# Kernel optimization log

Measured on AMD Instinct MI355X. Metric: run time of the kernel, lower is better.

The kernel has to match this reference:

```python
import jax, jax.numpy as jnp
import numpy as np

DIM = 1024
N_HEADS = 16
N_KV = 4
HEAD_DIM = 64
FFN = 4096
EPS = 1e-6
B, S = 2, 2048
ROPE_BASE = 10000.0


def rmsnorm(x, w, eps=EPS):
    ms = jnp.mean(jnp.square(x), axis=-1, keepdims=True)
    return x * jax.lax.rsqrt(ms + eps) * w


def apply_rotary(x, cos, sin):
    # x: [B,H,S,hd]; cos/sin: [S, hd//2] -> broadcast over B,H
    half = x.shape[-1] // 2
    x1, x2 = x[..., :half], x[..., half:]
    c = cos[None, None, :, :]
    s = sin[None, None, :, :]
    return jnp.concatenate((x1 * c + x2 * s, x2 * c - x1 * s), axis=-1)


def setup_inputs() -> dict:
    key = jax.random.key(0)
    ks = jax.random.split(key, 10)
    w = lambda k, shp: jax.random.normal(k, shp, dtype=jnp.float32) * 0.02
    pos = jnp.arange(S, dtype=jnp.float32)
    inv_freq = 1.0 / (ROPE_BASE ** (jnp.arange(0, HEAD_DIM // 2, dtype=jnp.float32) / (HEAD_DIM // 2)))
    ang = pos[:, None] * inv_freq[None, :]
    return {
        "x": jax.random.normal(ks[0], (B, S, DIM), dtype=jnp.float32),
        "w_norm1": jnp.ones((DIM,), jnp.float32),
        "wq": w(ks[1], (DIM, N_HEADS * HEAD_DIM)),
        "wk": w(ks[2], (DIM, N_KV * HEAD_DIM)),
        "wv": w(ks[3], (DIM, N_KV * HEAD_DIM)),
        "wo": w(ks[4], (N_HEADS * HEAD_DIM, DIM)),
        "attn_scale": jnp.ones((DIM,), jnp.float32),
        "w_norm2": jnp.ones((DIM,), jnp.float32),
        "wg": w(ks[5], (DIM, FFN)),
        "wu": w(ks[6], (DIM, FFN)),
        "wd": w(ks[7], (FFN, DIM)),
        "mlp_scale": jnp.ones((DIM,), jnp.float32),
        "cos": jnp.cos(ang),
        "sin": jnp.sin(ang),
    }


def block_forward(x, w_norm1, wq, wk, wv, wo, attn_scale, w_norm2, wg, wu, wd, mlp_scale, cos, sin):
    b, s, d = x.shape
    # ---- attention sub-block (pre-norm, RoPE, causal GQA SDPA, scaled residual) ----
    xn = rmsnorm(x, w_norm1)
    q = (xn @ wq).reshape(b, s, N_HEADS, HEAD_DIM).transpose(0, 2, 1, 3)  # [B,H,S,hd]
    k = (xn @ wk).reshape(b, s, N_KV, HEAD_DIM).transpose(0, 2, 1, 3)    # [B,KV,S,hd]
    v = (xn @ wv).reshape(b, s, N_KV, HEAD_DIM).transpose(0, 2, 1, 3)
    q = apply_rotary(q, cos, sin)
    k = apply_rotary(k, cos, sin)
    rep = N_HEADS // N_KV
    k = jnp.repeat(k, rep, axis=1)  # GQA expand -> [B,H,S,hd]
    v = jnp.repeat(v, rep, axis=1)
    scale = 1.0 / np.sqrt(HEAD_DIM)
    scores = jnp.einsum("bhqd,bhkd->bhqk", q, k) * scale
    causal = jnp.tril(jnp.ones((s, s), dtype=bool))
    scores = jnp.where(causal[None, None], scores, jnp.finfo(scores.dtype).min)
    probs = jax.nn.softmax(scores, axis=-1)
    attn = jnp.einsum("bhqk,bhkd->bhqd", probs, v)
    attn = attn.transpose(0, 2, 1, 3).reshape(b, s, N_HEADS * HEAD_DIM)
    x = x + (attn @ wo) * attn_scale[None, None, :]
    # ---- MLP sub-block (pre-norm, fused gate/up SwiGLU, down proj, scaled residual) ----
    xn2 = rmsnorm(x, w_norm2)
    hidden = jax.nn.silu(xn2 @ wg) * (xn2 @ wu)  # SwiGLU
    x = x + (hidden @ wd) * mlp_scale[None, None, :]
    return x


def reference(x, w_norm1, wq, wk, wv, wo, attn_scale, w_norm2, wg, wu, wd, mlp_scale, cos, sin):
    return block_forward(x, w_norm1, wq, wk, wv, wo, attn_scale, w_norm2, wg, wu, wd, mlp_scale, cos, sin)
```

## Files before the change

kernel.cpp:

```cpp
#include <hip/hip_runtime.h>
#include <hip/hip_bf16.h>
#include <cstdint>

typedef unsigned short u16;
typedef __attribute__((ext_vector_type(4))) float f32x4;
typedef __attribute__((ext_vector_type(8))) __bf16 bf16x8;

#define NH 16
#define NKV 4
#define SEQ 2048
#define NTOK 4096

__device__ inline u16 f2bf(float f) {
  return __builtin_bit_cast(u16, __float2bfloat16(f));
}
__device__ inline float bf2f(u16 u) {
  return __bfloat162float(__builtin_bit_cast(__hip_bfloat16, u));
}

#define GLDS(gp, lp) __builtin_amdgcn_global_load_lds( \
    (__attribute__((address_space(1))) void*)(gp), \
    (__attribute__((address_space(3))) void*)(lp), 16, 0, 0)

#define VMCNT0 asm volatile("s_waitcnt vmcnt(0)" ::: "memory")

__global__ __launch_bounds__(256) void rmsnorm_kernel(
    const float* __restrict__ x, const float* __restrict__ w,
    u16* __restrict__ out) {
  int row = blockIdx.x;
  int tid = threadIdx.x;
  const float4 v = reinterpret_cast<const float4*>(x + (size_t)row * 1024)[tid];
  float ss = v.x * v.x + v.y * v.y + v.z * v.z + v.w * v.w;
#pragma unroll
  for (int off = 32; off; off >>= 1) ss += __shfl_xor(ss, off);
  __shared__ float red[4];
  int lane = tid & 63, wid = tid >> 6;
  if (lane == 0) red[wid] = ss;
  __syncthreads();
  float tot = red[0] + red[1] + red[2] + red[3];
  float r = rsqrtf(tot * (1.0f / 1024.0f) + 1e-6f);
  const float4 wv = reinterpret_cast<const float4*>(w)[tid];
  ushort4 o;
  o.x = f2bf(v.x * r * wv.x);
  o.y = f2bf(v.y * r * wv.y);
  o.z = f2bf(v.z * r * wv.z);
  o.w = f2bf(v.w * r * wv.w);
  reinterpret_cast<ushort4*>(out + (size_t)row * 1024)[tid] = o;
}

__global__ __launch_bounds__(256) void transpose_cast_kernel(
    const float* __restrict__ src, u16* __restrict__ dst, int K, int N) {
  __shared__ float tile[32][33];
  int n0 = blockIdx.x * 32, k0 = blockIdx.y * 32;
  int tx = threadIdx.x & 31, ty = threadIdx.x >> 5;
#pragma unroll
  for (int i = 0; i < 4; i++)
    tile[ty + i * 8][tx] = src[(size_t)(k0 + ty + i * 8) * N + n0 + tx];
  __syncthreads();
#pragma unroll
  for (int i = 0; i < 4; i++)
    dst[(size_t)(n0 + ty + i * 8) * K + k0 + tx] = f2bf(tile[tx][ty + i * 8]);
}

template <int EP>
__device__ inline void epi_store(float v, size_t idx, int col,
                                 float* __restrict__ outf,
                                 const float* __restrict__ res,
                                 const float* __restrict__ scale,
                                 u16* __restrict__ outb) {
  if (EP == 0) {
    outf[idx] = v;
  } else if (EP == 1) {
    outf[idx] = res[idx] + v * scale[col];
  } else if (EP == 2) {
    outb[idx] = f2bf(v / (1.0f + __expf(-v)));
  } else {
    outb[idx] = f2bf(bf2f(outb[idx]) * v);
  }
}

template <int EP>
__global__ __launch_bounds__(512, 1) void gemmA(
    const u16* __restrict__ A, const u16* __restrict__ Bt,
    int M, int N, int K,
    float* __restrict__ outf, const float* __restrict__ res,
    const float* __restrict__ scale, u16* __restrict__ outb) {
  __shared__ u16 SA[2][256 * 64];
  __shared__ u16 SB[2][256 * 64];
  const int tid = threadIdx.x, lane = tid & 63, w = tid >> 6;
  const int wr = w >> 2, wc = w & 3;
  const int lg = lane >> 4, lc = lane & 15, cx = lc & 7;

  const int nbn = N >> 8;
  const int r8 = blockIdx.x & 7, j = blockIdx.x >> 3;
  const int bm = (((r8 >> 1) << 2) + (j & 3)) << 8;
  const int bn = ((r8 & 1) * (nbn >> 1) + (j >> 2)) << 8;

  const int swrow = lane >> 3;
  const int swcol = (lane & 7) ^ swrow;
  const u16* gA = A + (size_t)(bm + w * 16 + swrow) * K + swcol * 8;
  const u16* gB = Bt + (size_t)(bn + w * 16 + swrow) * K + swcol * 8;

  const int NT = K >> 6;
  f32x4 acc[8][4] = {};

#define SGA(T_) do { int sl_ = (T_) & 1; size_t ko_ = (size_t)(T_) * 64; \
    GLDS(gA + ko_,                    &SA[sl_][(w * 16) * 64]); \
    GLDS(gA + ko_ + (size_t)8 * K,    &SA[sl_][(w * 16 + 8) * 64]); \
    GLDS(gA + ko_ + (size_t)128 * K,  &SA[sl_][(128 + w * 16) * 64]); \
    GLDS(gA + ko_ + (size_t)136 * K,  &SA[sl_][(136 + w * 16) * 64]); } while (0)
#define SGB(T_) do { int sl_ = (T_) & 1; size_t ko_ = (size_t)(T_) * 64; \
    GLDS(gB + ko_,                    &SB[sl_][(w * 16) * 64]); \
    GLDS(gB + ko_ + (size_t)8 * K,    &SB[sl_][(w * 16 + 8) * 64]); \
    GLDS(gB + ko_ + (size_t)128 * K,  &SB[sl_][(128 + w * 16) * 64]); \
    GLDS(gB + ko_ + (size_t)136 * K,  &SB[sl_][(136 + w * 16) * 64]); } while (0)

  SGA(0);
  SGB(0);
  VMCNT0;
  __builtin_amdgcn_s_barrier();

  for (int t = 0; t < NT; ++t) {
    const u16* sa = &SA[t & 1][0];
    const u16* sb = &SB[t & 1][0];
    const bool more = (t + 1 < NT);

    bf16x8 bfr[4][2];
#pragma unroll
    for (int n = 0; n < 4; n++) {
      const int row = wc * 64 + n * 16 + lc;
#pragma unroll
      for (int ks = 0; ks < 2; ks++)
        bfr[n][ks] = *reinterpret_cast<const bf16x8*>(
            &sb[row * 64 + ((((ks << 2) | lg) ^ cx) << 3)]);
    }
    bf16x8 afr[4][2];
#pragma unroll
    for (int i = 0; i < 4; i++) {
      const int row = wr * 128 + i * 16 + lc;
#pragma unroll
      for (int ks = 0; ks < 2; ks++)
        afr[i][ks] = *reinterpret_cast<const bf16x8*>(
            &sa[row * 64 + ((((ks << 2) | lg) ^ cx) << 3)]);
    }
    if (more) SGA(t + 1);
    __builtin_amdgcn_s_setprio(1);
#pragma unroll
    for (int i = 0; i < 4; i++)
#pragma unroll
      for (int n = 0; n < 4; n++) {
        acc[i][n] = __builtin_amdgcn_mfma_f32_16x16x32_bf16(afr[i][0], bfr[n][0], acc[i][n], 0, 0, 0);
        acc[i][n] = __builtin_amdgcn_mfma_f32_16x16x32_bf16(afr[i][1], bfr[n][1], acc[i][n], 0, 0, 0);
      }
    __builtin_amdgcn_s_setprio(0);
#pragma unroll
    for (int i = 0; i < 4; i++) {
      const int row = wr * 128 + 64 + i * 16 + lc;
#pragma unroll
      for (int ks = 0; ks < 2; ks++)
        afr[i][ks] = *reinterpret_cast<const bf16x8*>(
            &sa[row * 64 + ((((ks << 2) | lg) ^ cx) << 3)]);
    }
    if (more) SGB(t + 1);
    __builtin_amdgcn_s_setprio(1);
#pragma unroll
    for (int i = 0; i < 4; i++)
#pragma unroll
      for (int n = 0; n < 4; n++) {
        acc[4 + i][n] = __builtin_amdgcn_mfma_f32_16x16x32_bf16(afr[i][0], bfr[n][0], acc[4 + i][n], 0, 0, 0);
        acc[4 + i][n] = __builtin_amdgcn_mfma_f32_16x16x32_bf16(afr[i][1], bfr[n][1], acc[4 + i][n], 0, 0, 0);
      }
    __builtin_amdgcn_s_setprio(0);
    VMCNT0;
    __builtin_amdgcn_s_barrier();
  }
#undef SGA
#undef SGB

#pragma unroll
  for (int mi = 0; mi < 8; mi++)
#pragma unroll
    for (int ni = 0; ni < 4; ni++)
#pragma unroll
      for (int rg = 0; rg < 4; rg++) {
        const int row = bm + wr * 128 + mi * 16 + lg * 4 + rg;
        const int col = bn + wc * 64 + ni * 16 + lc;
        epi_store<EP>(acc[mi][ni][rg], (size_t)row * N + col, col, outf, res, scale, outb);
      }
}

template <int EP>
__global__ __launch_bounds__(256, 1) void gemmB(
    const u16* __restrict__ A, const u16* __restrict__ Bt,
    int M, int N, int K,
    float* __restrict__ outf, const float* __restrict__ res,
    const float* __restrict__ scale, u16* __restrict__ outb) {
  __shared__ u16 SA[2][128 * 64];
  __shared__ u16 SB[2][128 * 64];
  const int tid = threadIdx.x, lane = tid & 63, w = tid >> 6;
  const int wr = w >> 1, wc = w & 1;
  const int lg = lane >> 4, lc = lane & 15, cx = lc & 7;

  const int r8 = blockIdx.x & 7, j = blockIdx.x >> 3;
  const int bm = ((r8 << 2) + (j & 3)) << 7;
  const int bn = (j >> 2) << 7;

  const int swrow = lane >> 3;
  const int swcol = (lane & 7) ^ swrow;
  const u16* gA = A + (size_t)(bm + w * 32 + swrow) * K + swcol * 8;
  const u16* gB = Bt + (size_t)(bn + w * 32 + swrow) * K + swcol * 8;

  const int NT = K >> 6;
  f32x4 acc[4][4] = {};

#define SG2(T_) do { int sl_ = (T_) & 1; size_t ko_ = (size_t)(T_) * 64; \
    GLDS(gA + ko_,                   &SA[sl_][(w * 32) * 64]); \
    GLDS(gA + ko_ + (size_t)8 * K,   &SA[sl_][(w * 32 + 8) * 64]); \
    GLDS(gA + ko_ + (size_t)16 * K,  &SA[sl_][(w * 32 + 16) * 64]); \
    GLDS(gA + ko_ + (size_t)24 * K,  &SA[sl_][(w * 32 + 24) * 64]); \
    GLDS(gB + ko_,                   &SB[sl_][(w * 32) * 64]); \
    GLDS(gB + ko_ + (size_t)8 * K,   &SB[sl_][(w * 32 + 8) * 64]); \
    GLDS(gB + ko_ + (size_t)16 * K,  &SB[sl_][(w * 32 + 16) * 64]); \
    GLDS(gB + ko_ + (size_t)24 * K,  &SB[sl_][(w * 32 + 24) * 64]); } while (0)

  SG2(0);
  VMCNT0;
  __builtin_amdgcn_s_barrier();

  for (int t = 0; t < NT; ++t) {
    const u16* sa = &SA[t & 1][0];
    const u16* sb = &SB[t & 1][0];
    const bool more = (t + 1 < NT);

    bf16x8 bfr[4][2], afr[4][2];
#pragma unroll
    for (int n = 0; n < 4; n++) {
      const int row = wc * 64 + n * 16 + lc;
#pragma unroll
      for (int ks = 0; ks < 2; ks++)
        bfr[n][ks] = *reinterpret_cast<const bf16x8*>(
            &sb[row * 64 + ((((ks << 2) | lg) ^ cx) << 3)]);
    }
#pragma unroll
    for (int i = 0; i < 4; i++) {
      const int row = wr * 64 + i * 16 + lc;
#pragma unroll
      for (int ks = 0; ks < 2; ks++)
        afr[i][ks] = *reinterpret_cast<const bf16x8*>(
            &sa[row * 64 + ((((ks << 2) | lg) ^ cx) << 3)]);
    }
    if (more) SG2(t + 1);
    __builtin_amdgcn_s_setprio(1);
#pragma unroll
    for (int i = 0; i < 4; i++)
#pragma unroll
      for (int n = 0; n < 4; n++) {
        acc[i][n] = __builtin_amdgcn_mfma_f32_16x16x32_bf16(afr[i][0], bfr[n][0], acc[i][n], 0, 0, 0);
        acc[i][n] = __builtin_amdgcn_mfma_f32_16x16x32_bf16(afr[i][1], bfr[n][1], acc[i][n], 0, 0, 0);
      }
    __builtin_amdgcn_s_setprio(0);
    VMCNT0;
    __builtin_amdgcn_s_barrier();
  }
#undef SG2

#pragma unroll
  for (int mi = 0; mi < 4; mi++)
#pragma unroll
    for (int ni = 0; ni < 4; ni++)
#pragma unroll
      for (int rg = 0; rg < 4; rg++) {
        const int row = bm + wr * 64 + mi * 16 + lg * 4 + rg;
        const int col = bn + wc * 64 + ni * 16 + lc;
        epi_store<EP>(acc[mi][ni][rg], (size_t)row * N + col, col, outf, res, scale, outb);
      }
}

__global__ __launch_bounds__(256) void rope_kernel(
    const float* __restrict__ qkv, const float* __restrict__ cosb,
    const float* __restrict__ sinb, u16* __restrict__ qr, u16* __restrict__ kr) {
  int idx = blockIdx.x * 256 + threadIdx.x;
  int d = idx & 31;
  int t = idx >> 5;
  int head = t % 20;
  int bs = t / 20;
  int s = bs & (SEQ - 1);
  int b = bs >> 11;
  const float* row = qkv + (size_t)bs * 1536;
  float c = cosb[s * 32 + d], sn = sinb[s * 32 + d];
  const float QSC = 0.18033688011112042f;
  float x1, x2;
  if (head < 16) {
    x1 = row[head * 64 + d];
    x2 = row[head * 64 + d + 32];
    size_t o = ((size_t)(b * NH + head) * SEQ + s) * 64 + d;
    qr[o] = f2bf((x1 * c + x2 * sn) * QSC);
    qr[o + 32] = f2bf((x2 * c - x1 * sn) * QSC);
  } else {
    int kh = head - 16;
    x1 = row[1024 + kh * 64 + d];
    x2 = row[1024 + kh * 64 + d + 32];
    size_t o = ((size_t)(b * NKV + kh) * SEQ + s) * 64 + d;
    kr[o] = f2bf(x1 * c + x2 * sn);
    kr[o + 32] = f2bf(x2 * c - x1 * sn);
  }
}

__global__ __launch_bounds__(256) void vtrans_kernel(
    const float* __restrict__ qkv, u16* __restrict__ vt) {
  int blk = blockIdx.x;
  int st = blk & 31; blk >>= 5;
  int kvh = blk & 3; blk >>= 2;
  int b = blk;
  __shared__ u16 tile[64][65];
  int tx = threadIdx.x & 63;
  int ty = threadIdx.x >> 6;
  int s0 = st * 64;
#pragma unroll
  for (int i = 0; i < 16; i++) {
    int sl = i * 4 + ty;
    tile[sl][tx] = f2bf(qkv[(size_t)(b * SEQ + s0 + sl) * 1536 + 1280 + kvh * 64 + tx]);
  }
  __syncthreads();
  size_t vbase = (size_t)(b * NKV + kvh) * 64 * SEQ;
#pragma unroll
  for (int i = 0; i < 16; i++) {
    int dd = i * 4 + ty;
    vt[vbase + (size_t)dd * SEQ + s0 + tx] = tile[tx][dd];
  }
}

__global__ __launch_bounds__(512, 1) void attn_kernel(
    const u16* __restrict__ qr, const u16* __restrict__ kr,
    const u16* __restrict__ vt, u16* __restrict__ out) {
  __shared__ u16 Ks[2][64 * 64];
  __shared__ u16 Vs[2][64 * 64];
  __shared__ u16 Ps[8][32 * 64];

  const int n = blockIdx.x;
  const int g = n & 7;
  const int b = g >> 2, kvh = g & 3;
  const int h = kvh * 4 + ((n >> 3) & 3);
  const int j = n >> 5;

  const int tid = threadIdx.x;
  const int lane = tid & 63, w = tid >> 6;
  const int lg = lane >> 4, lc = lane & 15;
  const int lc7 = lc & 7;

  const int isH = (w ^ (w >> 2)) & 1;
  const int strip = isH ? (15 - j) : j;
  const int q0w = strip * 128 + (w >> 1) * 32;
  const int nt = 2 * (15 - j) + 2;

  bf16x8 qf[2][2];
  {
    const u16* qp = qr + ((size_t)(b * NH + h) * SEQ + q0w + lc) * 64 + lg * 8;
#pragma unroll
    for (int qt = 0; qt < 2; qt++) {
      qf[qt][0] = *reinterpret_cast<const bf16x8*>(qp + qt * 16 * 64);
      qf[qt][1] = *reinterpret_cast<const bf16x8*>(qp + qt * 16 * 64 + 32);
    }
  }
  VMCNT0;

  const int srow = lane >> 3;
  const int scw = ((lane & 7) ^ srow) << 3;
  const u16* ksrc = kr + (size_t)(b * NKV + kvh) * SEQ * 64 + (size_t)(w * 8 + srow) * 64 + scw;
  const u16* vsrc = vt + ((size_t)(b * NKV + kvh) * 64 + w * 8 + srow) * SEQ + scw;
  u16* Pw = &Ps[w][0];

#define STAGEA(bufi, t) do { \
    GLDS(ksrc + (size_t)(t) * 64 * 64, &Ks[bufi][(w * 8) * 64]); \
    GLDS(vsrc + (size_t)(t) * 64,      &Vs[bufi][(w * 8) * 64]); \
  } while (0)

  STAGEA(0, 0);

  float mm[2] = {-1e30f, -1e30f}, ll[2] = {0.0f, 0.0f};
  f32x4 oacc[2][4] = {};

  int buf = 0;
  for (int t = 0; t < nt; ++t) {
    if (t + 1 < nt) {
      STAGEA(buf ^ 1, t + 1);
      asm volatile("s_waitcnt vmcnt(2)" ::: "memory");
    } else {
      VMCNT0;
    }
    __builtin_amdgcn_s_barrier();
    __builtin_amdgcn_sched_barrier(0);

    const int c0 = t * 64;
    if (c0 <= q0w + 31) {
      bf16x8 kf[4][2];
#pragma unroll
      for (int ni = 0; ni < 4; ni++) {
        const int row = ni * 16 + lc;
#pragma unroll
        for (int hf = 0; hf < 2; hf++)
          kf[ni][hf] = *reinterpret_cast<const bf16x8*>(
              &Ks[buf][row * 64 + ((((hf * 64 + lg * 16)) ^ (lc7 << 4)) >> 1)]);
      }
      f32x4 sc[4][2] = {};
      __builtin_amdgcn_s_setprio(1);
#pragma unroll
      for (int ni = 0; ni < 4; ni++)
#pragma unroll
        for (int qt = 0; qt < 2; qt++) {
          sc[ni][qt] = __builtin_amdgcn_mfma_f32_16x16x32_bf16(kf[ni][0], qf[qt][0], sc[ni][qt], 0, 0, 0);
          sc[ni][qt] = __builtin_amdgcn_mfma_f32_16x16x32_bf16(kf[ni][1], qf[qt][1], sc[ni][qt], 0, 0, 0);
        }
      __builtin_amdgcn_s_setprio(0);
      bf16x8 vf[4][2];
#pragma unroll
      for (int dt = 0; dt < 4; dt++) {
        const int row = dt * 16 + lc;
#pragma unroll
        for (int ks = 0; ks < 2; ks++)
          vf[dt][ks] = *reinterpret_cast<const bf16x8*>(
              &Vs[buf][row * 64 + (((ks * 64 + lg * 16) ^ (lc7 << 4)) >> 1)]);
      }
      if (c0 + 63 > q0w) {
#pragma unroll
        for (int qt = 0; qt < 2; qt++) {
          const int q = q0w + qt * 16 + lc;
#pragma unroll
          for (int ni = 0; ni < 4; ni++)
#pragma unroll
            for (int rg = 0; rg < 4; rg++)
              if (c0 + ni * 16 + lg * 4 + rg > q) sc[ni][qt][rg] = -1e30f;
        }
      }
      float mx[2];
#pragma unroll
      for (int qt = 0; qt < 2; qt++) {
        float v = -1e30f;
#pragma unroll
        for (int ni = 0; ni < 4; ni++)
#pragma unroll
          for (int rg = 0; rg < 4; rg++) v = fmaxf(v, sc[ni][qt][rg]);
        v = fmaxf(v, __shfl_xor(v, 16));
        v = fmaxf(v, __shfl_xor(v, 32));
        mx[qt] = v;
      }
      if (!__all(mx[0] - mm[0] <= 11.5f && mx[1] - mm[1] <= 11.5f)) {
        float al[2];
#pragma unroll
        for (int qt = 0; qt < 2; qt++) {
          float mn = fmaxf(mm[qt], mx[qt]);
          al[qt] = exp2f(mm[qt] - mn);
          mm[qt] = mn;
          ll[qt] *= al[qt];
        }
#pragma unroll
        for (int qt = 0; qt < 2; qt++)
#pragma unroll
          for (int rg = 0; rg < 4; rg++) {
            float a = __shfl(al[qt], lg * 4 + rg);
#pragma unroll
            for (int dt = 0; dt < 4; dt++) oacc[qt][dt][rg] *= a;
          }
      }
#pragma unroll
      for (int qt = 0; qt < 2; qt++) {
        float rs = 0.0f;
#pragma unroll
        for (int ni = 0; ni < 4; ni++)
#pragma unroll
          for (int rg = 0; rg < 4; rg++) {
            float p = exp2f(sc[ni][qt][rg] - mm[qt]);
            sc[ni][qt][rg] = p;
            rs += p;
          }
        rs += __shfl_xor(rs, 16);
        rs += __shfl_xor(rs, 32);
        ll[qt] += rs;
      }
#pragma unroll
      for (int qt = 0; qt < 2; qt++)
#pragma unroll
        for (int ni = 0; ni < 4; ni++) {
          ushort4 pk;
          pk.x = f2bf(sc[ni][qt][0]);
          pk.y = f2bf(sc[ni][qt][1]);
          pk.z = f2bf(sc[ni][qt][2]);
          pk.w = f2bf(sc[ni][qt][3]);
          *reinterpret_cast<ushort4*>(
              &Pw[(qt * 16 + lc) * 64 + (((ni * 32 + lg * 8) ^ (lc7 << 4)) >> 1)]) = pk;
        }
      __builtin_amdgcn_s_setprio(1);
#pragma unroll
      for (int qt = 0; qt < 2; qt++)
#pragma unroll
        for (int ks = 0; ks < 2; ks++) {
          bf16x8 pa = *reinterpret_cast<const bf16x8*>(
              &Pw[(qt * 16 + lc) * 64 + (((ks * 64 + lg * 16) ^ (lc7 << 4)) >> 1)]);
#pragma unroll
          for (int dt = 0; dt < 4; dt++)
            oacc[qt][dt] = __builtin_amdgcn_mfma_f32_16x16x32_bf16(pa, vf[dt][ks], oacc[qt][dt], 0, 0, 0);
        }
      __builtin_amdgcn_s_setprio(0);
    }
    asm volatile("s_waitcnt lgkmcnt(0)" ::: "memory");
    __builtin_amdgcn_s_barrier();
    __builtin_amdgcn_sched_barrier(0);
    buf ^= 1;
  }
#undef STAGEA

#pragma unroll
  for (int qt = 0; qt < 2; qt++) {
    const float li = 1.0f / ll[qt];
#pragma unroll
    for (int rg = 0; rg < 4; rg++) {
      float liq = __shfl(li, lg * 4 + rg);
      int q = q0w + qt * 16 + lg * 4 + rg;
      u16* orow = out + (size_t)(b * SEQ + q) * 1024 + h * 64 + lc;
#pragma unroll
      for (int dt = 0; dt < 4; dt++)
        orow[dt * 16] = f2bf(oacc[qt][dt][rg] * liq);
    }
  }
}

extern "C" void kernel_launch(void* const* d_in, const int* in_sizes, int n_in,
                              void* d_out, int out_size, void* d_ws, size_t ws_size,
                              hipStream_t stream) {
  const float* x = (const float*)d_in[0];
  const float* w_norm1 = (const float*)d_in[1];
  const float* wq = (const float*)d_in[2];
  const float* wk = (const float*)d_in[3];
  const float* wv = (const float*)d_in[4];
  const float* wo = (const float*)d_in[5];
  const float* attn_scale = (const float*)d_in[6];
  const float* w_norm2 = (const float*)d_in[7];
  const float* wg = (const float*)d_in[8];
  const float* wu = (const float*)d_in[9];
  const float* wd = (const float*)d_in[10];
  const float* mlp_scale = (const float*)d_in[11];
  const float* cosb = (const float*)d_in[12];
  const float* sinb = (const float*)d_in[13];
  float* out = (float*)d_out;

  char* ws = (char*)d_ws;
  u16* wqkv_t = (u16*)(ws + 0);
  u16* wo_t = (u16*)(ws + 3145728);
  u16* wg_t = (u16*)(ws + 5242880);
  u16* wu_t = (u16*)(ws + 13631488);
  u16* wd_t = (u16*)(ws + 22020096);
  u16* xn = (u16*)(ws + 30408704);
  float* qkv = (float*)(ws + 38797312);
  u16* attn_o = (u16*)(ws + 38797312);
  float* x1 = (float*)(ws + 47185920);
  u16* q_rope = (u16*)(ws + 63963136);
  u16* k_rope = (u16*)(ws + 72351744);
  u16* vt = (u16*)(ws + 74448896);
  u16* hbuf = (u16*)(ws + 63963136);

  dim3 tb(256);
  transpose_cast_kernel<<<dim3(32, 32), tb, 0, stream>>>(wq, wqkv_t, 1024, 1024);
  transpose_cast_kernel<<<dim3(8, 32), tb, 0, stream>>>(wk, wqkv_t + (size_t)1024 * 1024, 1024, 256);
  transpose_cast_kernel<<<dim3(8, 32), tb, 0, stream>>>(wv, wqkv_t + (size_t)1280 * 1024, 1024, 256);
  transpose_cast_kernel<<<dim3(32, 32), tb, 0, stream>>>(wo, wo_t, 1024, 1024);
  transpose_cast_kernel<<<dim3(128, 32), tb, 0, stream>>>(wg, wg_t, 1024, 4096);
  transpose_cast_kernel<<<dim3(128, 32), tb, 0, stream>>>(wu, wu_t, 1024, 4096);
  transpose_cast_kernel<<<dim3(32, 128), tb, 0, stream>>>(wd, wd_t, 4096, 1024);

  rmsnorm_kernel<<<4096, tb, 0, stream>>>(x, w_norm1, xn);
  gemmB<0><<<dim3(384), dim3(256), 0, stream>>>(xn, wqkv_t, 4096, 1536, 1024, qkv, nullptr, nullptr, nullptr);
  rope_kernel<<<10240, tb, 0, stream>>>(qkv, cosb, sinb, q_rope, k_rope);
  vtrans_kernel<<<2 * 4 * 32, tb, 0, stream>>>(qkv, vt);
  attn_kernel<<<256, dim3(512), 0, stream>>>(q_rope, k_rope, vt, attn_o);
  gemmB<1><<<dim3(256), dim3(256), 0, stream>>>(attn_o, wo_t, 4096, 1024, 1024, x1, x, attn_scale, nullptr);
  rmsnorm_kernel<<<4096, tb, 0, stream>>>(x1, w_norm2, xn);
  gemmA<2><<<dim3(256), dim3(512), 0, stream>>>(xn, wg_t, 4096, 4096, 1024, nullptr, nullptr, nullptr, hbuf);
  gemmA<3><<<dim3(256), dim3(512), 0, stream>>>(xn, wu_t, 4096, 4096, 1024, nullptr, nullptr, nullptr, hbuf);
  gemmB<1><<<dim3(256), dim3(256), 0, stream>>>(hbuf, wd_t, 4096, 1024, 4096, out, x1, mlp_scale, nullptr);
}
```

Baseline: 284.0 us.

## Switch attention to 32x32x16 MFMA and keep P in registers

Rewrites the attention inner loop to use 32x32x16 bf16 MFMA tiles instead of 16x16x32. With that tiling each lane owns a single query row, so the softmax state collapses to one max and one sum per lane. The probability matrix is repacked into the A-operand layout with cross-half lane shuffles, which removes the per-wave LDS scratch buffer and its write/read round trip. This trades LDS traffic and bank pressure for extra shuffles, more accumulator registers and a reworked mask and output index mapping that must match the MFMA layout exactly.

```diff
diff --git a/kernel.cpp b/kernel.cpp
--- a/kernel.cpp
+++ b/kernel.cpp
@@ -3,7 +3,9 @@
 #include <cstdint>
 
 typedef unsigned short u16;
+typedef unsigned int u32;
 typedef __attribute__((ext_vector_type(4))) float f32x4;
+typedef __attribute__((ext_vector_type(16))) float f32x16;
 typedef __attribute__((ext_vector_type(8))) __bf16 bf16x8;
 
 #define NH 16
@@ -16,6 +18,9 @@
 }
 __device__ inline float bf2f(u16 u) {
   return __bfloat162float(__builtin_bit_cast(__hip_bfloat16, u));
+}
+__device__ inline u32 pk2(float a, float b) {
+  return (u32)f2bf(a) | ((u32)f2bf(b) << 16);
 }
 
 #define GLDS(gp, lp) __builtin_amdgcn_global_load_lds( \
@@ -335,7 +340,6 @@
     const u16* __restrict__ vt, u16* __restrict__ out) {
   __shared__ u16 Ks[2][64 * 64];
   __shared__ u16 Vs[2][64 * 64];
-  __shared__ u16 Ps[8][32 * 64];
 
   const int n = blockIdx.x;
   const int g = n & 7;
@@ -345,22 +349,20 @@
 
   const int tid = threadIdx.x;
   const int lane = tid & 63, w = tid >> 6;
-  const int lg = lane >> 4, lc = lane & 15;
-  const int lc7 = lc & 7;
+  const int l31 = lane & 31, hi = lane >> 5;
 
   const int isH = (w ^ (w >> 2)) & 1;
   const int strip = isH ? (15 - j) : j;
   const int q0w = strip * 128 + (w >> 1) * 32;
+  const int qg = q0w + l31;
   const int nt = 2 * (15 - j) + 2;
 
-  bf16x8 qf[2][2];
+  bf16x8 qf[4];
   {
-    const u16* qp = qr + ((size_t)(b * NH + h) * SEQ + q0w + lc) * 64 + lg * 8;
-#pragma unroll
-    for (int qt = 0; qt < 2; qt++) {
-      qf[qt][0] = *reinterpret_cast<const bf16x8*>(qp + qt * 16 * 64);
-      qf[qt][1] = *reinterpret_cast<const bf16x8*>(qp + qt * 16 * 64 + 32);
-    }
+    const u16* qp = qr + ((size_t)(b * NH + h) * SEQ + qg) * 64 + 8 * hi;
+#pragma unroll
+    for (int c = 0; c < 4; c++)
+      qf[c] = *reinterpret_cast<const bf16x8*>(qp + 16 * c);
   }
   VMCNT0;
 
@@ -368,7 +370,6 @@
   const int scw = ((lane & 7) ^ srow) << 3;
   const u16* ksrc = kr + (size_t)(b * NKV + kvh) * SEQ * 64 + (size_t)(w * 8 + srow) * 64 + scw;
   const u16* vsrc = vt + ((size_t)(b * NKV + kvh) * 64 + w * 8 + srow) * SEQ + scw;
-  u16* Pw = &Ps[w][0];
 
 #define STAGEA(bufi, t) do { \
     GLDS(ksrc + (size_t)(t) * 64 * 64, &Ks[bufi][(w * 8) * 64]); \
@@ -377,8 +378,8 @@
 
   STAGEA(0, 0);
 
-  float mm[2] = {-1e30f, -1e30f}, ll[2] = {0.0f, 0.0f};
-  f32x4 oacc[2][4] = {};
+  float mm = -1e30f, ll = 0.0f;
+  f32x16 oacc[2] = {};
 
   int buf = 0;
   for (int t = 0; t < nt; ++t) {
@@ -393,113 +394,100 @@
 
     const int c0 = t * 64;
     if (c0 <= q0w + 31) {
-      bf16x8 kf[4][2];
-#pragma unroll
-      for (int ni = 0; ni < 4; ni++) {
-        const int row = ni * 16 + lc;
-#pragma unroll
-        for (int hf = 0; hf < 2; hf++)
-          kf[ni][hf] = *reinterpret_cast<const bf16x8*>(
-              &Ks[buf][row * 64 + ((((hf * 64 + lg * 16)) ^ (lc7 << 4)) >> 1)]);
-      }
-      f32x4 sc[4][2] = {};
+      f32x16 sc[2] = {};
       __builtin_amdgcn_s_setprio(1);
 #pragma unroll
-      for (int ni = 0; ni < 4; ni++)
-#pragma unroll
-        for (int qt = 0; qt < 2; qt++) {
-          sc[ni][qt] = __builtin_amdgcn_mfma_f32_16x16x32_bf16(kf[ni][0], qf[qt][0], sc[ni][qt], 0, 0, 0);
-          sc[ni][qt] = __builtin_amdgcn_mfma_f32_16x16x32_bf16(kf[ni][1], qf[qt][1], sc[ni][qt], 0, 0, 0);
+      for (int a = 0; a < 2; a++) {
+        const int row = a * 32 + l31;
+#pragma unroll
+        for (int c = 0; c < 4; c++) {
+          bf16x8 kf = *reinterpret_cast<const bf16x8*>(
+              &Ks[buf][row * 64 + (((2 * c + hi) ^ (row & 7)) << 3)]);
+          sc[a] = __builtin_amdgcn_mfma_f32_32x32x16_bf16(kf, qf[c], sc[a], 0, 0, 0);
         }
+      }
       __builtin_amdgcn_s_setprio(0);
-      bf16x8 vf[4][2];
-#pragma unroll
-      for (int dt = 0; dt < 4; dt++) {
-        const int row = dt * 16 + lc;
-#pragma unroll
-        for (int ks = 0; ks < 2; ks++)
-          vf[dt][ks] = *reinterpret_cast<const bf16x8*>(
-              &Vs[buf][row * 64 + (((ks * 64 + lg * 16) ^ (lc7 << 4)) >> 1)]);
-      }
+
+      bf16x8 vf[2][4];
+#pragma unroll
+      for (int dch = 0; dch < 2; dch++) {
+        const int row = dch * 32 + l31;
+#pragma unroll
+        for (int c = 0; c < 4; c++)
+          vf[dch][c] = *reinterpret_cast<const bf16x8*>(
+              &Vs[buf][row * 64 + (((2 * c + hi) ^ (row & 7)) << 3)]);
+      }
+
       if (c0 + 63 > q0w) {
 #pragma unroll
-        for (int qt = 0; qt < 2; qt++) {
-          const int q = q0w + qt * 16 + lc;
-#pragma unroll
-          for (int ni = 0; ni < 4; ni++)
-#pragma unroll
-            for (int rg = 0; rg < 4; rg++)
-              if (c0 + ni * 16 + lg * 4 + rg > q) sc[ni][qt][rg] = -1e30f;
+        for (int a = 0; a < 2; a++)
+#pragma unroll
+          for (int r = 0; r < 16; r++) {
+            const int key = c0 + 32 * a + (r & 3) + 8 * (r >> 2) + 4 * hi;
+            if (key > qg) sc[a][r] = -1e30f;
+          }
+      }
+
+      float mx = -1e30f;
+#pragma unroll
+      for (int a = 0; a < 2; a++)
+#pragma unroll
+        for (int r = 0; r < 16; r++) mx = fmaxf(mx, sc[a][r]);
+      mx = fmaxf(mx, __shfl_xor(mx, 32));
+
+      if (!__all(mx - mm <= 11.5f)) {
+        float mn = fmaxf(mm, mx);
+        float al = exp2f(mm - mn);
+        mm = mn;
+        ll *= al;
+#pragma unroll
+        for (int r = 0; r < 16; r++) {
+          float arr = __shfl(al, (r & 3) + 8 * (r >> 2) + 4 * hi);
+          oacc[0][r] *= arr;
+          oacc[1][r] *= arr;
         }
       }
-      float mx[2];
-#pragma unroll
-      for (int qt = 0; qt < 2; qt++) {
-        float v = -1e30f;
-#pragma unroll
-        for (int ni = 0; ni < 4; ni++)
-#pragma unroll
-          for (int rg = 0; rg < 4; rg++) v = fmaxf(v, sc[ni][qt][rg]);
-        v = fmaxf(v, __shfl_xor(v, 16));
-        v = fmaxf(v, __shfl_xor(v, 32));
-        mx[qt] = v;
-      }
-      if (!__all(mx[0] - mm[0] <= 11.5f && mx[1] - mm[1] <= 11.5f)) {
-        float al[2];
-#pragma unroll
-        for (int qt = 0; qt < 2; qt++) {
-          float mn = fmaxf(mm[qt], mx[qt]);
-          al[qt] = exp2f(mm[qt] - mn);
-          mm[qt] = mn;
-          ll[qt] *= al[qt];
+
+      float rs = 0.0f;
+#pragma unroll
+      for (int a = 0; a < 2; a++)
+#pragma unroll
+        for (int r = 0; r < 16; r++) {
+          float p = exp2f(sc[a][r] - mm);
+          sc[a][r] = p;
+          rs += p;
         }
-#pragma unroll
-        for (int qt = 0; qt < 2; qt++)
-#pragma unroll
-          for (int rg = 0; rg < 4; rg++) {
-            float a = __shfl(al[qt], lg * 4 + rg);
-#pragma unroll
-            for (int dt = 0; dt < 4; dt++) oacc[qt][dt][rg] *= a;
-          }
-      }
-#pragma unroll
-      for (int qt = 0; qt < 2; qt++) {
-        float rs = 0.0f;
-#pragma unroll
-        for (int ni = 0; ni < 4; ni++)
-#pragma unroll
-          for (int rg = 0; rg < 4; rg++) {
-            float p = exp2f(sc[ni][qt][rg] - mm[qt]);
-            sc[ni][qt][rg] = p;
-            rs += p;
-          }
-        rs += __shfl_xor(rs, 16);
-        rs += __shfl_xor(rs, 32);
-        ll[qt] += rs;
-      }
-#pragma unroll
-      for (int qt = 0; qt < 2; qt++)
-#pragma unroll
-        for (int ni = 0; ni < 4; ni++) {
-          ushort4 pk;
-          pk.x = f2bf(sc[ni][qt][0]);
-          pk.y = f2bf(sc[ni][qt][1]);
-          pk.z = f2bf(sc[ni][qt][2]);
-          pk.w = f2bf(sc[ni][qt][3]);
-          *reinterpret_cast<ushort4*>(
-              &Pw[(qt * 16 + lc) * 64 + (((ni * 32 + lg * 8) ^ (lc7 << 4)) >> 1)]) = pk;
-        }
+      rs += __shfl_xor(rs, 32);
+      ll += rs;
+
+      bf16x8 pa[4];
+#pragma unroll
+      for (int c = 0; c < 4; c++) {
+        const int a = c >> 1;
+        const int bb = 8 * (c & 1);
+        u32 A0 = pk2(sc[a][bb + 0], sc[a][bb + 1]);
+        u32 A1 = pk2(sc[a][bb + 2], sc[a][bb + 3]);
+        u32 B0 = pk2(sc[a][bb + 4], sc[a][bb + 5]);
+        u32 B1 = pk2(sc[a][bb + 6], sc[a][bb + 7]);
+        u32 s0 = hi ? A0 : B0;
+        u32 s1 = hi ? A1 : B1;
+        u32 r0 = (u32)__shfl_xor((int)s0, 32);
+        u32 r1 = (u32)__shfl_xor((int)s1, 32);
+        u32 w0 = hi ? r0 : A0;
+        u32 w1 = hi ? r1 : A1;
+        u32 w2 = hi ? B0 : r0;
+        u32 w3 = hi ? B1 : r1;
+        uint4 pw;
+        pw.x = w0; pw.y = w1; pw.z = w2; pw.w = w3;
+        pa[c] = __builtin_bit_cast(bf16x8, pw);
+      }
+
       __builtin_amdgcn_s_setprio(1);
 #pragma unroll
-      for (int qt = 0; qt < 2; qt++)
-#pragma unroll
-        for (int ks = 0; ks < 2; ks++) {
-          bf16x8 pa = *reinterpret_cast<const bf16x8*>(
-              &Pw[(qt * 16 + lc) * 64 + (((ks * 64 + lg * 16) ^ (lc7 << 4)) >> 1)]);
-#pragma unroll
-          for (int dt = 0; dt < 4; dt++)
-            oacc[qt][dt] = __builtin_amdgcn_mfma_f32_16x16x32_bf16(pa, vf[dt][ks], oacc[qt][dt], 0, 0, 0);
-        }
+      for (int c = 0; c < 4; c++) {
+        oacc[0] = __builtin_amdgcn_mfma_f32_32x32x16_bf16(pa[c], vf[0][c], oacc[0], 0, 0, 0);
+        oacc[1] = __builtin_amdgcn_mfma_f32_32x32x16_bf16(pa[c], vf[1][c], oacc[1], 0, 0, 0);
+      }
       __builtin_amdgcn_s_setprio(0);
     }
     asm volatile("s_waitcnt lgkmcnt(0)" ::: "memory");
@@ -509,18 +497,15 @@
   }
 #undef STAGEA
 
-#pragma unroll
-  for (int qt = 0; qt < 2; qt++) {
-    const float li = 1.0f / ll[qt];
-#pragma unroll
-    for (int rg = 0; rg < 4; rg++) {
-      float liq = __shfl(li, lg * 4 + rg);
-      int q = q0w + qt * 16 + lg * 4 + rg;
-      u16* orow = out + (size_t)(b * SEQ + q) * 1024 + h * 64 + lc;
-#pragma unroll
-      for (int dt = 0; dt < 4; dt++)
-        orow[dt * 16] = f2bf(oacc[qt][dt][rg] * liq);
-    }
+  const float li = 1.0f / ll;
+#pragma unroll
+  for (int r = 0; r < 16; r++) {
+    const int qloc = (r & 3) + 8 * (r >> 2) + 4 * hi;
+    float liq = __shfl(li, qloc);
+    const int q = q0w + qloc;
+    u16* orow = out + (size_t)(b * SEQ + q) * 1024 + h * 64 + l31;
+    orow[0] = f2bf(oacc[0][r] * liq);
+    orow[32] = f2bf(oacc[1][r] * liq);
   }
 }
 
```

After: 284.9 us. About the same (+0.3%).

## Fuse gate and up projections into one SwiGLU GEMM kernel

Applied to the files above, without the earlier changes.

Replaces the two separate gate and up GEMM launches, the second of which re-read and rewrote the bf16 hidden buffer, with one kernel that computes both accumulators from a shared A tile and applies SiLU(g)*u in the epilogue. This removes one full read of the activation matrix, the intermediate bf16 round-trip of the gate output, and one launch. Tiles change to 256x128 with K-step 32 and 2 blocks per CU, and each wave now holds two accumulator sets. The smaller K step doubles the barrier count per K, and register pressure may limit occupancy.

```diff
diff --git a/kernel.cpp b/kernel.cpp
--- a/kernel.cpp
+++ b/kernel.cpp
@@ -3,6 +3,7 @@
 #include <cstdint>
 
 typedef unsigned short u16;
+typedef unsigned int u32;
 typedef __attribute__((ext_vector_type(4))) float f32x4;
 typedef __attribute__((ext_vector_type(8))) __bf16 bf16x8;
 
@@ -80,116 +81,6 @@
 }
 
 template <int EP>
-__global__ __launch_bounds__(512, 1) void gemmA(
-    const u16* __restrict__ A, const u16* __restrict__ Bt,
-    int M, int N, int K,
-    float* __restrict__ outf, const float* __restrict__ res,
-    const float* __restrict__ scale, u16* __restrict__ outb) {
-  __shared__ u16 SA[2][256 * 64];
-  __shared__ u16 SB[2][256 * 64];
-  const int tid = threadIdx.x, lane = tid & 63, w = tid >> 6;
-  const int wr = w >> 2, wc = w & 3;
-  const int lg = lane >> 4, lc = lane & 15, cx = lc & 7;
-
-  const int nbn = N >> 8;
-  const int r8 = blockIdx.x & 7, j = blockIdx.x >> 3;
-  const int bm = (((r8 >> 1) << 2) + (j & 3)) << 8;
-  const int bn = ((r8 & 1) * (nbn >> 1) + (j >> 2)) << 8;
-
-  const int swrow = lane >> 3;
-  const int swcol = (lane & 7) ^ swrow;
-  const u16* gA = A + (size_t)(bm + w * 16 + swrow) * K + swcol * 8;
-  const u16* gB = Bt + (size_t)(bn + w * 16 + swrow) * K + swcol * 8;
-
-  const int NT = K >> 6;
-  f32x4 acc[8][4] = {};
-
-#define SGA(T_) do { int sl_ = (T_) & 1; size_t ko_ = (size_t)(T_) * 64; \
-    GLDS(gA + ko_,                    &SA[sl_][(w * 16) * 64]); \
-    GLDS(gA + ko_ + (size_t)8 * K,    &SA[sl_][(w * 16 + 8) * 64]); \
-    GLDS(gA + ko_ + (size_t)128 * K,  &SA[sl_][(128 + w * 16) * 64]); \
-    GLDS(gA + ko_ + (size_t)136 * K,  &SA[sl_][(136 + w * 16) * 64]); } while (0)
-#define SGB(T_) do { int sl_ = (T_) & 1; size_t ko_ = (size_t)(T_) * 64; \
-    GLDS(gB + ko_,                    &SB[sl_][(w * 16) * 64]); \
-    GLDS(gB + ko_ + (size_t)8 * K,    &SB[sl_][(w * 16 + 8) * 64]); \
-    GLDS(gB + ko_ + (size_t)128 * K,  &SB[sl_][(128 + w * 16) * 64]); \
-    GLDS(gB + ko_ + (size_t)136 * K,  &SB[sl_][(136 + w * 16) * 64]); } while (0)
-
-  SGA(0);
-  SGB(0);
-  VMCNT0;
-  __builtin_amdgcn_s_barrier();
-
-  for (int t = 0; t < NT; ++t) {
-    const u16* sa = &SA[t & 1][0];
-    const u16* sb = &SB[t & 1][0];
-    const bool more = (t + 1 < NT);
-
-    bf16x8 bfr[4][2];
-#pragma unroll
-    for (int n = 0; n < 4; n++) {
-      const int row = wc * 64 + n * 16 + lc;
-#pragma unroll
-      for (int ks = 0; ks < 2; ks++)
-        bfr[n][ks] = *reinterpret_cast<const bf16x8*>(
-            &sb[row * 64 + ((((ks << 2) | lg) ^ cx) << 3)]);
-    }
-    bf16x8 afr[4][2];
-#pragma unroll
-    for (int i = 0; i < 4; i++) {
-      const int row = wr * 128 + i * 16 + lc;
-#pragma unroll
-      for (int ks = 0; ks < 2; ks++)
-        afr[i][ks] = *reinterpret_cast<const bf16x8*>(
-            &sa[row * 64 + ((((ks << 2) | lg) ^ cx) << 3)]);
-    }
-    if (more) SGA(t + 1);
-    __builtin_amdgcn_s_setprio(1);
-#pragma unroll
-    for (int i = 0; i < 4; i++)
-#pragma unroll
-      for (int n = 0; n < 4; n++) {
-        acc[i][n] = __builtin_amdgcn_mfma_f32_16x16x32_bf16(afr[i][0], bfr[n][0], acc[i][n], 0, 0, 0);
-        acc[i][n] = __builtin_amdgcn_mfma_f32_16x16x32_bf16(afr[i][1], bfr[n][1], acc[i][n], 0, 0, 0);
-      }
-    __builtin_amdgcn_s_setprio(0);
-#pragma unroll
-    for (int i = 0; i < 4; i++) {
-      const int row = wr * 128 + 64 + i * 16 + lc;
-#pragma unroll
-      for (int ks = 0; ks < 2; ks++)
-        afr[i][ks] = *reinterpret_cast<const bf16x8*>(
-            &sa[row * 64 + ((((ks << 2) | lg) ^ cx) << 3)]);
-    }
-    if (more) SGB(t + 1);
-    __builtin_amdgcn_s_setprio(1);
-#pragma unroll
-    for (int i = 0; i < 4; i++)
-#pragma unroll
-      for (int n = 0; n < 4; n++) {
-        acc[4 + i][n] = __builtin_amdgcn_mfma_f32_16x16x32_bf16(afr[i][0], bfr[n][0], acc[4 + i][n], 0, 0, 0);
-        acc[4 + i][n] = __builtin_amdgcn_mfma_f32_16x16x32_bf16(afr[i][1], bfr[n][1], acc[4 + i][n], 0, 0, 0);
-      }
-    __builtin_amdgcn_s_setprio(0);
-    VMCNT0;
-    __builtin_amdgcn_s_barrier();
-  }
-#undef SGA
-#undef SGB
-
-#pragma unroll
-  for (int mi = 0; mi < 8; mi++)
-#pragma unroll
-    for (int ni = 0; ni < 4; ni++)
-#pragma unroll
-      for (int rg = 0; rg < 4; rg++) {
-        const int row = bm + wr * 128 + mi * 16 + lg * 4 + rg;
-        const int col = bn + wc * 64 + ni * 16 + lc;
-        epi_store<EP>(acc[mi][ni][rg], (size_t)row * N + col, col, outf, res, scale, outb);
-      }
-}
-
-template <int EP>
 __global__ __launch_bounds__(256, 1) void gemmB(
     const u16* __restrict__ A, const u16* __restrict__ Bt,
     int M, int N, int K,
@@ -273,6 +164,88 @@
         const int row = bm + wr * 64 + mi * 16 + lg * 4 + rg;
         const int col = bn + wc * 64 + ni * 16 + lc;
         epi_store<EP>(acc[mi][ni][rg], (size_t)row * N + col, col, outf, res, scale, outb);
+      }
+}
+
+__global__ __launch_bounds__(512, 2) void gateup_kernel(
+    const u16* __restrict__ A, const u16* __restrict__ Bg,
+    const u16* __restrict__ Bu, u16* __restrict__ outb) {
+  const int K = 1024, N = 4096;
+  __shared__ u16 SA[2][256 * 32];
+  __shared__ u16 SG[2][128 * 32];
+  __shared__ u16 SU[2][128 * 32];
+  const int tid = threadIdx.x, lane = tid & 63, w = tid >> 6;
+  const int wr = w >> 1, wc = w & 1;
+  const int lg = lane >> 4, lc = lane & 15;
+
+  const int r8 = blockIdx.x & 7, j = blockIdx.x >> 3;
+  const int bm = (((r8 >> 1) << 2) + (j & 3)) << 8;
+  const int bn = ((r8 & 1) * 16 + (j >> 2)) << 7;
+
+  const int srow = tid >> 2;
+  const int scs = ((tid & 3) ^ (srow & 3)) * 8;
+  const u16* gAs = A + (size_t)(bm + srow) * K + scs;
+  const u16* gGs = Bg + (size_t)(bn + srow) * K + scs;
+  const u16* gUs = Bu + (size_t)(bn + srow) * K + scs;
+
+  f32x4 accG[4][4] = {}, accU[4][4] = {};
+
+#define SGU(T_) do { int sl_ = (T_) & 1; size_t ko_ = (size_t)(T_) * 32; \
+    GLDS(gAs + ko_,                   &SA[sl_][w * 512]); \
+    GLDS(gAs + ko_ + (size_t)128 * K, &SA[sl_][4096 + w * 512]); \
+    GLDS(gGs + ko_,                   &SG[sl_][w * 512]); \
+    GLDS(gUs + ko_,                   &SU[sl_][w * 512]); } while (0)
+
+  SGU(0);
+  VMCNT0;
+  __builtin_amdgcn_s_barrier();
+
+  for (int t = 0; t < 32; ++t) {
+    const u16* sa = &SA[t & 1][0];
+    const u16* sg = &SG[t & 1][0];
+    const u16* su = &SU[t & 1][0];
+    const bool more = (t + 1 < 32);
+
+    bf16x8 afr[4], gfr[4], ufr[4];
+#pragma unroll
+    for (int i = 0; i < 4; i++) {
+      const int row = wr * 64 + i * 16 + lc;
+      afr[i] = *reinterpret_cast<const bf16x8*>(
+          &sa[row * 32 + ((lg ^ (lc & 3)) << 3)]);
+    }
+#pragma unroll
+    for (int n = 0; n < 4; n++) {
+      const int row = wc * 64 + n * 16 + lc;
+      const int off = row * 32 + ((lg ^ (lc & 3)) << 3);
+      gfr[n] = *reinterpret_cast<const bf16x8*>(&sg[off]);
+      ufr[n] = *reinterpret_cast<const bf16x8*>(&su[off]);
+    }
+    if (more) SGU(t + 1);
+    __builtin_amdgcn_s_setprio(1);
+#pragma unroll
+    for (int i = 0; i < 4; i++)
+#pragma unroll
+      for (int n = 0; n < 4; n++) {
+        accG[i][n] = __builtin_amdgcn_mfma_f32_16x16x32_bf16(afr[i], gfr[n], accG[i][n], 0, 0, 0);
+        accU[i][n] = __builtin_amdgcn_mfma_f32_16x16x32_bf16(afr[i], ufr[n], accU[i][n], 0, 0, 0);
+      }
+    __builtin_amdgcn_s_setprio(0);
+    VMCNT0;
+    __builtin_amdgcn_s_barrier();
+  }
+#undef SGU
+
+#pragma unroll
+  for (int mi = 0; mi < 4; mi++)
+#pragma unroll
+    for (int ni = 0; ni < 4; ni++)
+#pragma unroll
+      for (int rg = 0; rg < 4; rg++) {
+        const int row = bm + wr * 64 + mi * 16 + lg * 4 + rg;
+        const int col = bn + wc * 64 + ni * 16 + lc;
+        const float g = accG[mi][ni][rg];
+        const float u = accU[mi][ni][rg];
+        outb[(size_t)row * N + col] = f2bf((g / (1.0f + __expf(-g))) * u);
       }
 }
 
@@ -574,7 +547,6 @@
   attn_kernel<<<256, dim3(512), 0, stream>>>(q_rope, k_rope, vt, attn_o);
   gemmB<1><<<dim3(256), dim3(256), 0, stream>>>(attn_o, wo_t, 4096, 1024, 1024, x1, x, attn_scale, nullptr);
   rmsnorm_kernel<<<4096, tb, 0, stream>>>(x1, w_norm2, xn);
-  gemmA<2><<<dim3(256), dim3(512), 0, stream>>>(xn, wg_t, 4096, 4096, 1024, nullptr, nullptr, nullptr, hbuf);
-  gemmA<3><<<dim3(256), dim3(512), 0, stream>>>(xn, wu_t, 4096, 4096, 1024, nullptr, nullptr, nullptr, hbuf);
+  gateup_kernel<<<dim3(512), dim3(512), 0, stream>>>(xn, wg_t, wu_t, hbuf);
   gemmB<1><<<dim3(256), dim3(256), 0, stream>>>(hbuf, wd_t, 4096, 1024, 4096, out, x1, mlp_scale, nullptr);
 }
```

New measurement: 266.7 us. -6.1%, faster.
